# Kernel optimization log

Hardware: AMD Instinct MI355X
Metric: run time of the kernel (lower is better)

The kernel has to match this reference:

```python
import jax, jax.numpy as jnp
import numpy as np

D_MODEL = 1024
D_FF = 4096
NUM_EXPERTS = 8
TOP_K = 2
LN_EPS = 1e-5


def setup_inputs() -> dict:
    key = jax.random.key(0)
    ks = jax.random.split(key, 12)
    B, S, D, F, E = 4, 2048, D_MODEL, D_FF, NUM_EXPERTS
    s = 0.02
    return {
        "x": jax.random.normal(ks[0], (B, S, D), jnp.float32),
        # gating network: Linear(D, D//2) -> ReLU -> Linear(D//2, E)
        "gw1": jax.random.normal(ks[1], (D, D // 2), jnp.float32) * s,
        "gb1": jnp.zeros((D // 2,), jnp.float32),
        "gw2": jax.random.normal(ks[2], (D // 2, E), jnp.float32) * s,
        "gb2": jnp.zeros((E,), jnp.float32),
        # stacked expert FFNs: Linear(D,F) -> GELU -> Linear(F,D), then *scale + bias
        "we1": jax.random.normal(ks[3], (E, D, F), jnp.float32) * s,
        "be1": jnp.zeros((E, F), jnp.float32),
        "we2": jax.random.normal(ks[4], (E, F, D), jnp.float32) * s,
        "be2": jnp.zeros((E, D), jnp.float32),
        "escale": jnp.ones((E, D), jnp.float32),
        "ebias": jax.random.normal(ks[5], (E, D), jnp.float32) * 0.01,
        # output LayerNorm
        "gamma": jnp.ones((D,), jnp.float32),
        "beta": jnp.zeros((D,), jnp.float32),
    }


def _layernorm(x, gamma, beta):
    mu = jnp.mean(x, axis=-1, keepdims=True)
    var = jnp.mean(jnp.square(x - mu), axis=-1, keepdims=True)
    return (x - mu) * jax.lax.rsqrt(var + LN_EPS) * gamma + beta


def reference(x, gw1, gb1, gw2, gb2, we1, be1, we2, be2, escale, ebias, gamma, beta):
    B, S, D = x.shape
    xf = x.reshape(-1, D)  # [T, D]

    # ---- gating (eval mode: no noise, no dropout) ----
    gate_logits = jax.nn.relu(xf @ gw1 + gb1) @ gw2 + gb2  # [T, E]
    top_v, top_i = jax.lax.top_k(gate_logits, TOP_K)       # [T, K]
    gates = jax.nn.softmax(top_v, axis=-1)                 # [T, K]

    # load balancing loss: KL( uniform || mean softmax probs ), sum reduction
    probs = jax.nn.softmax(gate_logits, axis=-1)
    expert_probs = probs.mean(axis=0)                      # [E]
    t = 1.0 / NUM_EXPERTS
    load_loss = jnp.sum(t * (jnp.log(t) - jnp.log(expert_probs + 1e-8)))

    # ---- dense compute over ALL experts (faithful to source) ----
    h = jnp.einsum('td,edf->tef', xf, we1) + be1           # [T, E, F]
    h = jax.nn.gelu(h, approximate=False)                  # nn.GELU default = erf
    eo = jnp.einsum('tef,efd->ted', h, we2) + be2          # [T, E, D]
    eo = eo * escale + ebias                               # per-expert scale/bias

    # ---- top-k gather + weighted combine ----
    sel = jnp.take_along_axis(eo, top_i[:, :, None], axis=1)  # [T, K, D]
    out = jnp.sum(gates[:, :, None] * sel, axis=1)            # [T, D]

    y = _layernorm(x + out.reshape(B, S, D), gamma, beta)
    return y, load_loss
```

## Files before the change

kernel.cpp:

```cpp
#include <hip/hip_runtime.h>
#include <hip/hip_bf16.h>
#include <math.h>

#define T_TOK 8192
#define DM    1024
#define DFF   4096
#define NE    8
#define DH    512
#define NSLOT (T_TOK*2)
#define MAXT  136

typedef float  f32x4  __attribute__((ext_vector_type(4)));
typedef __bf16 bf16x8 __attribute__((ext_vector_type(8)));

__device__ inline ushort f2bf(float f) {
  union { float f; unsigned int u; } v; v.f = f;
  unsigned int r = (v.u + 0x7FFFu + ((v.u >> 16) & 1u)) >> 16;
  return (ushort)r;
}

__device__ inline float bf2f(ushort u) {
  union { unsigned int i; float f; } v; v.i = ((unsigned int)u) << 16; return v.f;
}

__device__ __forceinline__ float gelu_erf(float v) {
  float xx = v * 0.70710678118654752f;
  float ax = fabsf(xx);
  float t  = __builtin_amdgcn_rcpf(1.f + 0.3275911f * ax);
  float p  = t * (0.254829592f + t * (-0.284496736f + t * (1.421413741f +
             t * (-1.453152027f + t * 1.061405429f))));
  float er = 1.f - p * __expf(-ax * ax);
  er = copysignf(er, xx);
  return 0.5f * v * (1.f + er);
}

__device__ inline void gl_lds16(const void* g, void* l) {
  __builtin_amdgcn_global_load_lds(
      (const __attribute__((address_space(1))) unsigned int*)g,
      (__attribute__((address_space(3))) unsigned int*)l, 16, 0, 0);
}

__global__ void k_init(int* counts, int* fill, float* psum) {
  int i = threadIdx.x;
  if (i < NE) { counts[i] = 0; fill[i] = 0; psum[i] = 0.f; }
}

__global__ void k_cvt_x(const float* __restrict__ x, ushort* __restrict__ xh,
                        ushort* __restrict__ xl, int n4) {
  int i = blockIdx.x * blockDim.x + threadIdx.x;
  int st = gridDim.x * blockDim.x;
  for (; i < n4; i += st) {
    float4 v = ((const float4*)x)[i];
    ushort4 h, l;
    h.x = f2bf(v.x); l.x = f2bf(v.x - bf2f(h.x));
    h.y = f2bf(v.y); l.y = f2bf(v.y - bf2f(h.y));
    h.z = f2bf(v.z); l.z = f2bf(v.z - bf2f(h.z));
    h.w = f2bf(v.w); l.w = f2bf(v.w - bf2f(h.w));
    ((ushort4*)xh)[i] = h;
    ((ushort4*)xl)[i] = l;
  }
}

__global__ __launch_bounds__(256) void k_tr(const float* __restrict__ in,
                                            ushort* __restrict__ out, int R, int C) {
  __shared__ float tile[64][65];
  int e = blockIdx.z;
  in  += (size_t)e * R * C;
  out += (size_t)e * R * C;
  int r0 = blockIdx.y * 64, c0 = blockIdx.x * 64;
  int tx = threadIdx.x & 63, ty = threadIdx.x >> 6;
  for (int i = 0; i < 16; i++) {
    int r = ty + i * 4;
    tile[r][tx] = in[(size_t)(r0 + r) * C + c0 + tx];
  }
  __syncthreads();
  for (int i = 0; i < 16; i++) {
    int c = ty + i * 4;
    out[(size_t)(c0 + c) * R + r0 + tx] = f2bf(tile[tx][c]);
  }
}

__global__ __launch_bounds__(256) void k_trg(const float* __restrict__ in,
                                             ushort* __restrict__ outh,
                                             ushort* __restrict__ outl) {
  __shared__ float tile[64][65];
  int r0 = blockIdx.y * 64, c0 = blockIdx.x * 64;
  int tx = threadIdx.x & 63, ty = threadIdx.x >> 6;
  for (int i = 0; i < 16; i++) {
    int r = ty + i * 4;
    tile[r][tx] = in[(size_t)(r0 + r) * DH + c0 + tx];
  }
  __syncthreads();
  for (int i = 0; i < 16; i++) {
    int c = ty + i * 4;
    float f = tile[tx][c];
    ushort h = f2bf(f);
    outh[(size_t)(c0 + c) * DM + r0 + tx] = h;
    outl[(size_t)(c0 + c) * DM + r0 + tx] = f2bf(f - bf2f(h));
  }
}

__global__ __launch_bounds__(256) void k_gate1m(const ushort* __restrict__ xh,
                                                const ushort* __restrict__ xl,
                                                const ushort* __restrict__ w1ht,
                                                const ushort* __restrict__ w1lt,
                                                const float* __restrict__ b,
                                                float* __restrict__ g1) {
  constexpr int GX = DH / 128;
  constexpr int NWG = GX * (T_TOK / 128);
  int id = blockIdx.y * GX + blockIdx.x;
  int wg = (id & 7) * (NWG / 8) + (id >> 3);
  int m0 = (wg / GX) * 128;
  int n0 = (wg % GX) * 128;

  __shared__ ushort lds[2][16384];

  int t = threadIdx.x;
  int wave = t >> 6, lane = t & 63;
  int wr = wave >> 1, wc = wave & 1;

  int r = t >> 2;
  int csrc = (((t & 3) ^ ((t >> 3) & 3)) * 8);
  const ushort* ah0 = xh + (size_t)(m0 + r) * DM + csrc;
  const ushort* ah1 = xh + (size_t)(m0 + r + 64) * DM + csrc;
  const ushort* al0 = xl + (size_t)(m0 + r) * DM + csrc;
  const ushort* al1 = xl + (size_t)(m0 + r + 64) * DM + csrc;
  const ushort* bh0 = w1ht + (size_t)(n0 + r) * DM + csrc;
  const ushort* bh1 = w1ht + (size_t)(n0 + r + 64) * DM + csrc;
  const ushort* bl0 = w1lt + (size_t)(n0 + r) * DM + csrc;
  const ushort* bl1 = w1lt + (size_t)(n0 + r + 64) * DM + csrc;

  auto stage = [&](int b_, int k0) {
    ushort* base = lds[b_];
    gl_lds16(ah0 + k0, base + t * 8);
    gl_lds16(ah1 + k0, base + (t + 256) * 8);
    gl_lds16(al0 + k0, base + 4096 + t * 8);
    gl_lds16(al1 + k0, base + 4096 + (t + 256) * 8);
    gl_lds16(bh0 + k0, base + 8192 + t * 8);
    gl_lds16(bh1 + k0, base + 8192 + (t + 256) * 8);
    gl_lds16(bl0 + k0, base + 12288 + t * 8);
    gl_lds16(bl1 + k0, base + 12288 + (t + 256) * 8);
  };

  f32x4 acc[4][4] = {};
  int la = lane & 15;
  int kqs = (((lane >> 4) ^ ((la >> 1) & 3)) * 8);
  constexpr int NT = DM / 32;

  stage(0, 0);
  stage(1, 32);
  for (int kt = 0; kt < NT; kt++) {
    if (kt + 1 < NT) asm volatile("s_waitcnt vmcnt(8)" ::: "memory");
    else             asm volatile("s_waitcnt vmcnt(0)" ::: "memory");
    __builtin_amdgcn_s_barrier();
    const ushort* bb = lds[kt & 1];
    bf16x8 fah[4], fal[4], fbh[4], fbl[4];
#pragma unroll
    for (int m = 0; m < 4; m++) {
      int ro = (wr * 64 + m * 16 + la) * 32 + kqs;
      fah[m] = *(const bf16x8*)&bb[ro];
      fal[m] = *(const bf16x8*)&bb[4096 + ro];
    }
#pragma unroll
    for (int n = 0; n < 4; n++) {
      int ro = (wc * 64 + n * 16 + la) * 32 + kqs;
      fbh[n] = *(const bf16x8*)&bb[8192 + ro];
      fbl[n] = *(const bf16x8*)&bb[12288 + ro];
    }
    asm volatile("s_waitcnt lgkmcnt(0)" ::: "memory");
    __builtin_amdgcn_s_barrier();
    if (kt + 2 < NT) stage(kt & 1, (kt + 2) * 32);
#pragma unroll
    for (int m = 0; m < 4; m++)
#pragma unroll
      for (int n = 0; n < 4; n++)
        acc[m][n] = __builtin_amdgcn_mfma_f32_16x16x32_bf16(fah[m], fbh[n], acc[m][n], 0, 0, 0);
#pragma unroll
    for (int m = 0; m < 4; m++)
#pragma unroll
      for (int n = 0; n < 4; n++)
        acc[m][n] = __builtin_amdgcn_mfma_f32_16x16x32_bf16(fah[m], fbl[n], acc[m][n], 0, 0, 0);
#pragma unroll
    for (int m = 0; m < 4; m++)
#pragma unroll
      for (int n = 0; n < 4; n++)
        acc[m][n] = __builtin_amdgcn_mfma_f32_16x16x32_bf16(fal[m], fbh[n], acc[m][n], 0, 0, 0);
  }

#pragma unroll
  for (int m = 0; m < 4; m++) {
    int rbase = m0 + wr * 64 + m * 16 + ((lane >> 4) << 2);
#pragma unroll
    for (int n = 0; n < 4; n++) {
      int c = n0 + wc * 64 + n * 16 + la;
      float bv = b[c];
      f32x4 a = acc[m][n];
#pragma unroll
      for (int j = 0; j < 4; j++)
        g1[(size_t)(rbase + j) * DH + c] = fmaxf(a[j] + bv, 0.f);
    }
  }
}

__global__ __launch_bounds__(256) void k_gate2(const float* __restrict__ g1,
                                               const float* __restrict__ w2,
                                               const float* __restrict__ b2,
                                               float* __restrict__ logits) {
  int wave = threadIdx.x >> 6, lane = threadIdx.x & 63;
  int tok = blockIdx.x * 4 + wave;
  const float* row = &g1[(size_t)tok * DH];
  float v[8];
#pragma unroll
  for (int j = 0; j < 8; j++) v[j] = row[lane + 64 * j];
  float acc[8];
#pragma unroll
  for (int e = 0; e < NE; e++) {
    float s = 0.f;
#pragma unroll
    for (int j = 0; j < 8; j++) s += v[j] * w2[(size_t)(lane + 64 * j) * NE + e];
    acc[e] = s;
  }
  for (int off = 32; off > 0; off >>= 1)
#pragma unroll
    for (int e = 0; e < NE; e++) acc[e] += __shfl_down(acc[e], off);
  if (lane == 0)
#pragma unroll
    for (int e = 0; e < NE; e++) logits[(size_t)tok * NE + e] = acc[e] + b2[e];
}

__global__ __launch_bounds__(256) void k_route(const float* __restrict__ logits,
                                               int* __restrict__ topi,
                                               float* __restrict__ gatesw,
                                               int* __restrict__ counts,
                                               float* __restrict__ psum) {
  int t = blockIdx.x * blockDim.x + threadIdx.x;
  const float* lp = &logits[(size_t)t * NE];
  float l[8];
#pragma unroll
  for (int e = 0; e < NE; e++) l[e] = lp[e];
  int i0 = 0; float v0 = l[0];
#pragma unroll
  for (int e = 1; e < NE; e++) if (l[e] > v0) { v0 = l[e]; i0 = e; }
  int i1 = (i0 == 0) ? 1 : 0; float v1 = l[i1];
#pragma unroll
  for (int e = 0; e < NE; e++)
    if (e != i0 && l[e] > v1) { v1 = l[e]; i1 = e; }
  float g0 = 1.f / (1.f + expf(v1 - v0));
  topi[t * 2] = i0; topi[t * 2 + 1] = i1;
  gatesw[t * 2] = g0; gatesw[t * 2 + 1] = 1.f - g0;
  float p[8]; float s = 0.f;
#pragma unroll
  for (int e = 0; e < NE; e++) { p[e] = expf(l[e] - v0); s += p[e]; }
  float inv = 1.f / s;
  int lane = threadIdx.x & 63;
#pragma unroll
  for (int e = 0; e < NE; e++) {
    float pe = p[e] * inv;
    for (int off = 32; off > 0; off >>= 1) pe += __shfl_down(pe, off);
    if (lane == 0) atomicAdd(&psum[e], pe);
  }
#pragma unroll
  for (int e = 0; e < NE; e++) {
    unsigned long long m0 = __ballot(i0 == e);
    unsigned long long m1 = __ballot(i1 == e);
    if (lane == 0) {
      int c = __popcll(m0) + __popcll(m1);
      if (c) atomicAdd(&counts[e], c);
    }
  }
}

__global__ void k_scan(const int* __restrict__ counts, int* __restrict__ offsets,
                       const float* __restrict__ psum, float* __restrict__ loss_out,
                       int* __restrict__ tile_e, int* __restrict__ tile_mt) {
  if (threadIdx.x == 0) {
    int off = 0;
    for (int e = 0; e < NE; e++) { offsets[e] = off; off += counts[e]; }
    offsets[NE] = off;
    float tt = 1.f / NE, loss = 0.f;
    for (int e = 0; e < NE; e++) {
      float pe = psum[e] / (float)T_TOK;
      loss += tt * (logf(tt) - logf(pe + 1e-8f));
    }
    loss_out[0] = loss;
    int n = 0;
    for (int e = 0; e < NE; e++) {
      int rows = counts[e];
      for (int mt = 0; mt * 128 < rows; mt++) { tile_e[n] = e; tile_mt[n] = mt; n++; }
    }
    for (int i = n; i < MAXT; i++) { tile_e[i] = -1; tile_mt[i] = 0; }
  }
}

__global__ __launch_bounds__(256) void k_fill(const int* __restrict__ topi,
                                              const int* __restrict__ offsets,
                                              int* __restrict__ fill,
                                              int* __restrict__ slot_tok,
                                              int* __restrict__ tok_slot) {
  int t = blockIdx.x * blockDim.x + threadIdx.x;
  for (int k = 0; k < 2; k++) {
    int e = topi[t * 2 + k];
    int pos = offsets[e] + atomicAdd(&fill[e], 1);
    slot_tok[pos] = t;
    tok_slot[t * 2 + k] = pos;
  }
}

__global__ __launch_bounds__(256, 3) void k_egemm1(const ushort* __restrict__ xb,
                                                   const ushort* __restrict__ w1t,
                                                   const float* __restrict__ be1,
                                                   const int* __restrict__ slot_tok,
                                                   const int* __restrict__ offsets,
                                                   const int* __restrict__ tile_e,
                                                   const int* __restrict__ tile_mt,
                                                   ushort* __restrict__ H) {
  constexpr int GX = DFF / 128;
  constexpr int NWG = GX * MAXT;
  int id = blockIdx.y * GX + blockIdx.x;
  int wg = (id & 7) * (NWG / 8) + (id >> 3);
  int ty = wg / GX;
  int n0 = (wg % GX) * 128;
  int e = tile_e[ty];
  if (e < 0) return;
  int mt = tile_mt[ty];
  int beg = offsets[e], nrows = offsets[e + 1] - beg;
  const ushort* B = w1t + (size_t)e * DFF * DM;

  __shared__ ushort As[2][4096];
  __shared__ ushort Bs[2][4096];

  int t = threadIdx.x;
  int wave = t >> 6, lane = t & 63;
  int wr = wave >> 1, wc = wave & 1;

  int r_g0 = mt * 128 + (t >> 2);
  int r_g1 = r_g0 + 64;
  int tok0 = slot_tok[beg + (r_g0 < nrows ? r_g0 : 0)];
  int tok1 = slot_tok[beg + (r_g1 < nrows ? r_g1 : 0)];
  int acol = (((t & 3) ^ ((t >> 3) & 3)) * 8);
  const ushort* aptr0 = xb + (size_t)tok0 * DM + acol;
  const ushort* aptr1 = xb + (size_t)tok1 * DM + acol;
  const ushort* bptr0 = B + (size_t)(n0 + (t >> 2)) * DM + acol;
  const ushort* bptr1 = B + (size_t)(n0 + (t >> 2) + 64) * DM + acol;
  char* adst = (char*)As + t * 16;
  char* bdst = (char*)Bs + t * 16;

  auto stage = [&](int b, int k0) {
    gl_lds16(aptr0 + k0, adst + b * 8192);
    gl_lds16(aptr1 + k0, adst + b * 8192 + 4096);
    gl_lds16(bptr0 + k0, bdst + b * 8192);
    gl_lds16(bptr1 + k0, bdst + b * 8192 + 4096);
  };

  f32x4 acc[4][4] = {};
  int la = lane & 15;
  int kqs = (((lane >> 4) ^ ((la >> 1) & 3)) * 8);
  constexpr int NT = DM / 32;

  stage(0, 0);
  stage(1, 32);
  for (int kt = 0; kt < NT; kt++) {
    if (kt + 1 < NT) asm volatile("s_waitcnt vmcnt(4)" ::: "memory");
    else             asm volatile("s_waitcnt vmcnt(0)" ::: "memory");
    __builtin_amdgcn_s_barrier();
    const ushort* Ab = As[kt & 1];
    const ushort* Bb = Bs[kt & 1];
    bf16x8 af[4], bfr[4];
#pragma unroll
    for (int m = 0; m < 4; m++)
      af[m] = *(const bf16x8*)&Ab[(wr * 64 + m * 16 + la) * 32 + kqs];
#pragma unroll
    for (int n = 0; n < 4; n++)
      bfr[n] = *(const bf16x8*)&Bb[(wc * 64 + n * 16 + la) * 32 + kqs];
    asm volatile("s_waitcnt lgkmcnt(0)" ::: "memory");
    __builtin_amdgcn_s_barrier();
    if (kt + 2 < NT) stage(kt & 1, (kt + 2) * 32);
#pragma unroll
    for (int m = 0; m < 4; m++)
#pragma unroll
      for (int n = 0; n < 4; n++)
        acc[m][n] = __builtin_amdgcn_mfma_f32_16x16x32_bf16(af[m], bfr[n], acc[m][n], 0, 0, 0);
  }

  int row0 = mt * 128 + wr * 64;
  int c_of = n0 + wc * 64;
#pragma unroll
  for (int m = 0; m < 4; m++) {
    int rbase = row0 + m * 16 + ((lane >> 4) << 2);
#pragma unroll
    for (int n = 0; n < 4; n++) {
      int c = c_of + n * 16 + la;
      float b1 = be1[e * DFF + c];
      f32x4 a = acc[m][n];
#pragma unroll
      for (int j = 0; j < 4; j++) {
        int rr = rbase + j;
        if (rr < nrows) {
          float v = a[j] + b1;
          H[(size_t)(beg + rr) * DFF + c] = f2bf(gelu_erf(v));
        }
      }
    }
  }
}

__global__ __launch_bounds__(256, 3) void k_egemm2(const ushort* __restrict__ H,
                                                   const ushort* __restrict__ w2t,
                                                   const float* __restrict__ be2,
                                                   const float* __restrict__ escale,
                                                   const float* __restrict__ ebias,
                                                   const int* __restrict__ offsets,
                                                   const int* __restrict__ tile_e,
                                                   const int* __restrict__ tile_mt,
                                                   ushort* __restrict__ eo) {
  constexpr int GX = DM / 128;
  constexpr int NWG = GX * MAXT;
  int id = blockIdx.y * GX + blockIdx.x;
  int wg = (id & 7) * (NWG / 8) + (id >> 3);
  int ty = wg / GX;
  int n0 = (wg % GX) * 128;
  int e = tile_e[ty];
  if (e < 0) return;
  int mt = tile_mt[ty];
  int beg = offsets[e], nrows = offsets[e + 1] - beg;
  const ushort* B = w2t + (size_t)e * DM * DFF;

  __shared__ ushort As[2][4096];
  __shared__ ushort Bs[2][4096];

  int t = threadIdx.x;
  int wave = t >> 6, lane = t & 63;
  int wr = wave >> 1, wc = wave & 1;

  int r_g0 = mt * 128 + (t >> 2);
  int r_g1 = r_g0 + 64;
  int s0 = beg + (r_g0 < nrows ? r_g0 : 0);
  int s1 = beg + (r_g1 < nrows ? r_g1 : 0);
  int acol = (((t & 3) ^ ((t >> 3) & 3)) * 8);
  const ushort* aptr0 = H + (size_t)s0 * DFF + acol;
  const ushort* aptr1 = H + (size_t)s1 * DFF + acol;
  const ushort* bptr0 = B + (size_t)(n0 + (t >> 2)) * DFF + acol;
  const ushort* bptr1 = B + (size_t)(n0 + (t >> 2) + 64) * DFF + acol;
  char* adst = (char*)As + t * 16;
  char* bdst = (char*)Bs + t * 16;

  auto stage = [&](int b, int k0) {
    gl_lds16(aptr0 + k0, adst + b * 8192);
    gl_lds16(aptr1 + k0, adst + b * 8192 + 4096);
    gl_lds16(bptr0 + k0, bdst + b * 8192);
    gl_lds16(bptr1 + k0, bdst + b * 8192 + 4096);
  };

  f32x4 acc[4][4] = {};
  int la = lane & 15;
  int kqs = (((lane >> 4) ^ ((la >> 1) & 3)) * 8);
  constexpr int NT = DFF / 32;

  stage(0, 0);
  stage(1, 32);
  for (int kt = 0; kt < NT; kt++) {
    if (kt + 1 < NT) asm volatile("s_waitcnt vmcnt(4)" ::: "memory");
    else             asm volatile("s_waitcnt vmcnt(0)" ::: "memory");
    __builtin_amdgcn_s_barrier();
    const ushort* Ab = As[kt & 1];
    const ushort* Bb = Bs[kt & 1];
    bf16x8 af[4], bfr[4];
#pragma unroll
    for (int m = 0; m < 4; m++)
      af[m] = *(const bf16x8*)&Ab[(wr * 64 + m * 16 + la) * 32 + kqs];
#pragma unroll
    for (int n = 0; n < 4; n++)
      bfr[n] = *(const bf16x8*)&Bb[(wc * 64 + n * 16 + la) * 32 + kqs];
    asm volatile("s_waitcnt lgkmcnt(0)" ::: "memory");
    __builtin_amdgcn_s_barrier();
    if (kt + 2 < NT) stage(kt & 1, (kt + 2) * 32);
#pragma unroll
    for (int m = 0; m < 4; m++)
#pragma unroll
      for (int n = 0; n < 4; n++)
        acc[m][n] = __builtin_amdgcn_mfma_f32_16x16x32_bf16(af[m], bfr[n], acc[m][n], 0, 0, 0);
  }

  int row0 = mt * 128 + wr * 64;
  int c_of = n0 + wc * 64;
#pragma unroll
  for (int m = 0; m < 4; m++) {
    int rbase = row0 + m * 16 + ((lane >> 4) << 2);
#pragma unroll
    for (int n = 0; n < 4; n++) {
      int c = c_of + n * 16 + la;
      float b2 = be2[e * DM + c];
      float sc = escale[e * DM + c];
      float bb = ebias[e * DM + c];
      f32x4 a = acc[m][n];
#pragma unroll
      for (int j = 0; j < 4; j++) {
        int rr = rbase + j;
        if (rr < nrows) {
          float v = (a[j] + b2) * sc + bb;
          eo[(size_t)(beg + rr) * DM + c] = f2bf(v);
        }
      }
    }
  }
}

__global__ __launch_bounds__(256) void k_ln(const float* __restrict__ x,
                                            const ushort* __restrict__ eo,
                                            const int* __restrict__ tok_slot,
                                            const float* __restrict__ gatesw,
                                            const float* __restrict__ gamma,
                                            const float* __restrict__ beta,
                                            float* __restrict__ y) {
  int t = blockIdx.x;
  int s0 = tok_slot[t * 2], s1 = tok_slot[t * 2 + 1];
  float g0 = gatesw[t * 2], g1 = gatesw[t * 2 + 1];
  const float* xr = &x[(size_t)t * DM];
  const ushort* e0 = &eo[(size_t)s0 * DM];
  const ushort* e1 = &eo[(size_t)s1 * DM];
  int tid = threadIdx.x;
  int c0 = tid * 4;
  float4 xv = *(const float4*)&xr[c0];
  ushort4 a0 = *(const ushort4*)&e0[c0];
  ushort4 a1 = *(const ushort4*)&e1[c0];
  float v[4];
  v[0] = xv.x + g0 * bf2f(a0.x) + g1 * bf2f(a1.x);
  v[1] = xv.y + g0 * bf2f(a0.y) + g1 * bf2f(a1.y);
  v[2] = xv.z + g0 * bf2f(a0.z) + g1 * bf2f(a1.z);
  v[3] = xv.w + g0 * bf2f(a0.w) + g1 * bf2f(a1.w);
  float sum = v[0] + v[1] + v[2] + v[3];
  __shared__ float red[4];
  __shared__ float red2[4];
  for (int off = 32; off > 0; off >>= 1) sum += __shfl_down(sum, off);
  if ((tid & 63) == 0) red[tid >> 6] = sum;
  __syncthreads();
  float mu = (red[0] + red[1] + red[2] + red[3]) * (1.f / DM);
  float vs = 0.f;
#pragma unroll
  for (int i = 0; i < 4; i++) { float d = v[i] - mu; vs += d * d; }
  for (int off = 32; off > 0; off >>= 1) vs += __shfl_down(vs, off);
  if ((tid & 63) == 0) red2[tid >> 6] = vs;
  __syncthreads();
  float var = (red2[0] + red2[1] + red2[2] + red2[3]) * (1.f / DM);
  float rs = rsqrtf(var + 1e-5f);
  float4 gm = *(const float4*)&gamma[c0];
  float4 bt = *(const float4*)&beta[c0];
  float4 o;
  o.x = (v[0] - mu) * rs * gm.x + bt.x;
  o.y = (v[1] - mu) * rs * gm.y + bt.y;
  o.z = (v[2] - mu) * rs * gm.z + bt.z;
  o.w = (v[3] - mu) * rs * gm.w + bt.w;
  *(float4*)&y[(size_t)t * DM + c0] = o;
}

extern "C" void kernel_launch(void* const* d_in, const int* in_sizes, int n_in,
                              void* d_out, int out_size, void* d_ws, size_t ws_size,
                              hipStream_t stream) {
  const float* x    = (const float*)d_in[0];
  const float* gw1  = (const float*)d_in[1];
  const float* gb1  = (const float*)d_in[2];
  const float* gw2  = (const float*)d_in[3];
  const float* gb2  = (const float*)d_in[4];
  const float* we1  = (const float*)d_in[5];
  const float* be1  = (const float*)d_in[6];
  const float* we2  = (const float*)d_in[7];
  const float* be2  = (const float*)d_in[8];
  const float* escale = (const float*)d_in[9];
  const float* ebias  = (const float*)d_in[10];
  const float* gamma  = (const float*)d_in[11];
  const float* beta   = (const float*)d_in[12];
  float* y = (float*)d_out;
  float* loss_out = y + (size_t)T_TOK * DM;

  char* w = (char*)d_ws;
  ushort* xh    = (ushort*)w; w += (size_t)T_TOK * DM * 2;
  ushort* xl    = (ushort*)w; w += (size_t)T_TOK * DM * 2;
  ushort* w1t   = (ushort*)w; w += (size_t)NE * DFF * DM * 2;
  ushort* w2t   = (ushort*)w; w += (size_t)NE * DM * DFF * 2;
  ushort* H     = (ushort*)w; w += (size_t)NSLOT * DFF * 2;
  ushort* eo    = (ushort*)w; w += (size_t)NSLOT * DM * 2;
  ushort* w1ht  = (ushort*)w; w += (size_t)DH * DM * 2;
  ushort* w1lt  = (ushort*)w; w += (size_t)DH * DM * 2;
  float* g1     = (float*)w;  w += (size_t)T_TOK * DH * 4;
  float* logits = (float*)w;  w += (size_t)T_TOK * NE * 4;
  int*   topi   = (int*)w;    w += (size_t)T_TOK * 2 * 4;
  float* gatesw = (float*)w;  w += (size_t)T_TOK * 2 * 4;
  int* slot_tok = (int*)w;    w += (size_t)NSLOT * 4;
  int* tok_slot = (int*)w;    w += (size_t)T_TOK * 2 * 4;
  int* counts   = (int*)w;    w += 64;
  int* fill     = (int*)w;    w += 64;
  int* offsets  = (int*)w;    w += 64;
  float* psum   = (float*)w;  w += 64;
  int* tile_e   = (int*)w;    w += MAXT * 4 + 32;
  int* tile_mt  = (int*)w;    w += MAXT * 4 + 32;

  k_init<<<1, 64, 0, stream>>>(counts, fill, psum);
  k_cvt_x<<<2048, 256, 0, stream>>>(x, xh, xl, T_TOK * DM / 4);
  k_trg<<<dim3(8, 16), 256, 0, stream>>>(gw1, w1ht, w1lt);
  k_tr<<<dim3(64, 16, 8), 256, 0, stream>>>(we1, w1t, DM, DFF);
  k_tr<<<dim3(16, 64, 8), 256, 0, stream>>>(we2, w2t, DFF, DM);
  k_gate1m<<<dim3(DH / 128, T_TOK / 128), 256, 0, stream>>>(xh, xl, w1ht, w1lt, gb1, g1);
  k_gate2<<<T_TOK / 4, 256, 0, stream>>>(g1, gw2, gb2, logits);
  k_route<<<T_TOK / 256, 256, 0, stream>>>(logits, topi, gatesw, counts, psum);
  k_scan<<<1, 64, 0, stream>>>(counts, offsets, psum, loss_out, tile_e, tile_mt);
  k_fill<<<T_TOK / 256, 256, 0, stream>>>(topi, offsets, fill, slot_tok, tok_slot);
  k_egemm1<<<dim3(DFF / 128, MAXT), 256, 0, stream>>>(xh, w1t, be1, slot_tok, offsets,
                                                      tile_e, tile_mt, H);
  k_egemm2<<<dim3(DM / 128, MAXT), 256, 0, stream>>>(H, w2t, be2, escale, ebias,
                                                     offsets, tile_e, tile_mt, eo);
  k_ln<<<T_TOK, 256, 0, stream>>>(x, eo, tok_slot, gatesw, gamma, beta, y);
}
```

Baseline: 688.8 us.

## Enlarge expert GEMM1 tiles, triple-buffer LDS, vectorize transposes, fold init kernel

The first expert GEMM now uses 256x256 tiles with 512 threads and a separate coarser tile schedule, which raises operand reuse per workgroup. Both expert GEMMs move to a three-stage LDS ring with a single barrier per k-step and raise wave priority around the MFMA block. The weight-transpose kernel now uses float4 loads and ushort4 stores, and the counter-init kernel is folded into the x conversion kernel to save a launch. In exchange, GEMM1 has fewer workgroups, more registers per thread and a larger LDS footprint, which may lower occupancy and waste more work on padded rows.

Measured after the change: 754.2 us. 1.09x slower.

```diff
diff --git a/kernel.cpp b/kernel.cpp
--- a/kernel.cpp
+++ b/kernel.cpp
@@ -9,6 +9,7 @@
 #define DH    512
 #define NSLOT (T_TOK*2)
 #define MAXT  136
+#define MAXT2 72
 
 typedef float  f32x4  __attribute__((ext_vector_type(4)));
 typedef __bf16 bf16x8 __attribute__((ext_vector_type(8)));
@@ -40,13 +41,14 @@
       (__attribute__((address_space(3))) unsigned int*)l, 16, 0, 0);
 }
 
-__global__ void k_init(int* counts, int* fill, float* psum) {
-  int i = threadIdx.x;
-  if (i < NE) { counts[i] = 0; fill[i] = 0; psum[i] = 0.f; }
-}
+#define SBAR  __builtin_amdgcn_s_barrier()
 
 __global__ void k_cvt_x(const float* __restrict__ x, ushort* __restrict__ xh,
-                        ushort* __restrict__ xl, int n4) {
+                        ushort* __restrict__ xl, int n4,
+                        int* counts, int* fill, float* psum) {
+  if (blockIdx.x == 0 && threadIdx.x < NE) {
+    counts[threadIdx.x] = 0; fill[threadIdx.x] = 0; psum[threadIdx.x] = 0.f;
+  }
   int i = blockIdx.x * blockDim.x + threadIdx.x;
   int st = gridDim.x * blockDim.x;
   for (; i < n4; i += st) {
@@ -68,15 +70,25 @@
   in  += (size_t)e * R * C;
   out += (size_t)e * R * C;
   int r0 = blockIdx.y * 64, c0 = blockIdx.x * 64;
-  int tx = threadIdx.x & 63, ty = threadIdx.x >> 6;
-  for (int i = 0; i < 16; i++) {
-    int r = ty + i * 4;
-    tile[r][tx] = in[(size_t)(r0 + r) * C + c0 + tx];
+  int t = threadIdx.x;
+  int lr = t >> 4, lc = (t & 15) * 4;
+#pragma unroll
+  for (int i = 0; i < 4; i++) {
+    int r = lr + i * 16;
+    float4 v = *(const float4*)&in[(size_t)(r0 + r) * C + c0 + lc];
+    tile[r][lc] = v.x; tile[r][lc + 1] = v.y; tile[r][lc + 2] = v.z; tile[r][lc + 3] = v.w;
   }
   __syncthreads();
-  for (int i = 0; i < 16; i++) {
-    int c = ty + i * 4;
-    out[(size_t)(c0 + c) * R + r0 + tx] = f2bf(tile[tx][c]);
+  int g = t & 15, cc = t >> 4;
+#pragma unroll
+  for (int i = 0; i < 4; i++) {
+    int c = cc + i * 16;
+    ushort4 o;
+    o.x = f2bf(tile[g * 4 + 0][c]);
+    o.y = f2bf(tile[g * 4 + 1][c]);
+    o.z = f2bf(tile[g * 4 + 2][c]);
+    o.w = f2bf(tile[g * 4 + 3][c]);
+    *(ushort4*)&out[(size_t)(c0 + c) * R + r0 + g * 4] = o;
   }
 }
 
@@ -272,7 +284,8 @@
 
 __global__ void k_scan(const int* __restrict__ counts, int* __restrict__ offsets,
                        const float* __restrict__ psum, float* __restrict__ loss_out,
-                       int* __restrict__ tile_e, int* __restrict__ tile_mt) {
+                       int* __restrict__ tile_e, int* __restrict__ tile_mt,
+                       int* __restrict__ tile_e2, int* __restrict__ tile_mt2) {
   if (threadIdx.x == 0) {
     int off = 0;
     for (int e = 0; e < NE; e++) { offsets[e] = off; off += counts[e]; }
@@ -289,6 +302,12 @@
       for (int mt = 0; mt * 128 < rows; mt++) { tile_e[n] = e; tile_mt[n] = mt; n++; }
     }
     for (int i = n; i < MAXT; i++) { tile_e[i] = -1; tile_mt[i] = 0; }
+    n = 0;
+    for (int e = 0; e < NE; e++) {
+      int rows = counts[e];
+      for (int mt = 0; mt * 256 < rows; mt++) { tile_e2[n] = e; tile_mt2[n] = mt; n++; }
+    }
+    for (int i = n; i < MAXT2; i++) { tile_e2[i] = -1; tile_mt2[i] = 0; }
   }
 }
 
@@ -306,99 +325,97 @@
   }
 }
 
-__global__ __launch_bounds__(256, 3) void k_egemm1(const ushort* __restrict__ xb,
+__global__ __launch_bounds__(512, 2) void k_egemm1(const ushort* __restrict__ xb,
                                                    const ushort* __restrict__ w1t,
                                                    const float* __restrict__ be1,
                                                    const int* __restrict__ slot_tok,
                                                    const int* __restrict__ offsets,
-                                                   const int* __restrict__ tile_e,
-                                                   const int* __restrict__ tile_mt,
+                                                   const int* __restrict__ tile_e2,
+                                                   const int* __restrict__ tile_mt2,
                                                    ushort* __restrict__ H) {
-  constexpr int GX = DFF / 128;
-  constexpr int NWG = GX * MAXT;
+  constexpr int GX = DFF / 256;
+  constexpr int NWG = GX * MAXT2;
+  constexpr int NT = DM / 32;
   int id = blockIdx.y * GX + blockIdx.x;
   int wg = (id & 7) * (NWG / 8) + (id >> 3);
   int ty = wg / GX;
-  int n0 = (wg % GX) * 128;
-  int e = tile_e[ty];
+  int n0c = (wg % GX) * 256;
+  int e = tile_e2[ty];
   if (e < 0) return;
-  int mt = tile_mt[ty];
+  int mt = tile_mt2[ty];
   int beg = offsets[e], nrows = offsets[e + 1] - beg;
-  const ushort* B = w1t + (size_t)e * DFF * DM;
-
-  __shared__ ushort As[2][4096];
-  __shared__ ushort Bs[2][4096];
+  const ushort* Bw = w1t + (size_t)e * DFF * DM;
+
+  __shared__ ushort As[3][8192];
+  __shared__ ushort Bs[3][8192];
 
   int t = threadIdx.x;
-  int wave = t >> 6, lane = t & 63;
-  int wr = wave >> 1, wc = wave & 1;
-
-  int r_g0 = mt * 128 + (t >> 2);
-  int r_g1 = r_g0 + 64;
-  int tok0 = slot_tok[beg + (r_g0 < nrows ? r_g0 : 0)];
-  int tok1 = slot_tok[beg + (r_g1 < nrows ? r_g1 : 0)];
-  int acol = (((t & 3) ^ ((t >> 3) & 3)) * 8);
-  const ushort* aptr0 = xb + (size_t)tok0 * DM + acol;
-  const ushort* aptr1 = xb + (size_t)tok1 * DM + acol;
-  const ushort* bptr0 = B + (size_t)(n0 + (t >> 2)) * DM + acol;
-  const ushort* bptr1 = B + (size_t)(n0 + (t >> 2) + 64) * DM + acol;
+  int lane = t & 63, la = lane & 15, lh = lane >> 4;
+  int wid = t >> 6, wm = wid >> 2, wn = wid & 3;
+
+  int csrc = (((t & 3) ^ ((t >> 3) & 3)) * 8);
+  auto arow = [&](int r) {
+    r = mt * 256 + r; if (r >= nrows) r = nrows - 1;
+    return (size_t)slot_tok[beg + r];
+  };
+  int rr0 = t >> 2;
+  const ushort* aptr0 = xb + arow(rr0) * DM + csrc;
+  const ushort* aptr1 = xb + arow(128 + rr0) * DM + csrc;
+  const ushort* bptr0 = Bw + (size_t)(n0c + rr0) * DM + csrc;
+  const ushort* bptr1 = Bw + (size_t)(n0c + 128 + rr0) * DM + csrc;
   char* adst = (char*)As + t * 16;
   char* bdst = (char*)Bs + t * 16;
 
   auto stage = [&](int b, int k0) {
-    gl_lds16(aptr0 + k0, adst + b * 8192);
-    gl_lds16(aptr1 + k0, adst + b * 8192 + 4096);
-    gl_lds16(bptr0 + k0, bdst + b * 8192);
-    gl_lds16(bptr1 + k0, bdst + b * 8192 + 4096);
+    gl_lds16(aptr0 + k0, adst + b * 16384);
+    gl_lds16(aptr1 + k0, adst + b * 16384 + 8192);
+    gl_lds16(bptr0 + k0, bdst + b * 16384);
+    gl_lds16(bptr1 + k0, bdst + b * 16384 + 8192);
   };
 
-  f32x4 acc[4][4] = {};
-  int la = lane & 15;
+  f32x4 acc[8][4] = {};
   int kqs = (((lane >> 4) ^ ((la >> 1) & 3)) * 8);
-  constexpr int NT = DM / 32;
 
   stage(0, 0);
   stage(1, 32);
+  asm volatile("s_waitcnt vmcnt(4)" ::: "memory");
+  SBAR;
   for (int kt = 0; kt < NT; kt++) {
-    if (kt + 1 < NT) asm volatile("s_waitcnt vmcnt(4)" ::: "memory");
-    else             asm volatile("s_waitcnt vmcnt(0)" ::: "memory");
-    __builtin_amdgcn_s_barrier();
-    const ushort* Ab = As[kt & 1];
-    const ushort* Bb = Bs[kt & 1];
-    bf16x8 af[4], bfr[4];
-#pragma unroll
-    for (int m = 0; m < 4; m++)
-      af[m] = *(const bf16x8*)&Ab[(wr * 64 + m * 16 + la) * 32 + kqs];
+    if (kt + 2 < NT) stage((kt + 2) % 3, (kt + 2) * 32);
+    const ushort* Ab = As[kt % 3];
+    const ushort* Bb = Bs[kt % 3];
+    bf16x8 af[8], bfr[4];
+#pragma unroll
+    for (int m = 0; m < 8; m++)
+      af[m] = *(const bf16x8*)&Ab[(wm * 128 + m * 16 + la) * 32 + kqs];
 #pragma unroll
     for (int n = 0; n < 4; n++)
-      bfr[n] = *(const bf16x8*)&Bb[(wc * 64 + n * 16 + la) * 32 + kqs];
+      bfr[n] = *(const bf16x8*)&Bb[(wn * 64 + n * 16 + la) * 32 + kqs];
     asm volatile("s_waitcnt lgkmcnt(0)" ::: "memory");
-    __builtin_amdgcn_s_barrier();
-    if (kt + 2 < NT) stage(kt & 1, (kt + 2) * 32);
-#pragma unroll
-    for (int m = 0; m < 4; m++)
+    __builtin_amdgcn_s_setprio(1);
+#pragma unroll
+    for (int m = 0; m < 8; m++)
 #pragma unroll
       for (int n = 0; n < 4; n++)
         acc[m][n] = __builtin_amdgcn_mfma_f32_16x16x32_bf16(af[m], bfr[n], acc[m][n], 0, 0, 0);
-  }
-
-  int row0 = mt * 128 + wr * 64;
-  int c_of = n0 + wc * 64;
-#pragma unroll
-  for (int m = 0; m < 4; m++) {
-    int rbase = row0 + m * 16 + ((lane >> 4) << 2);
+    __builtin_amdgcn_s_setprio(0);
+    if (kt + 2 < NT)      { asm volatile("s_waitcnt vmcnt(4)" ::: "memory"); SBAR; }
+    else if (kt + 1 < NT) { asm volatile("s_waitcnt vmcnt(0)" ::: "memory"); SBAR; }
+  }
+
+#pragma unroll
+  for (int m = 0; m < 8; m++) {
+    int lrow = mt * 256 + wm * 128 + m * 16 + lh * 4;
 #pragma unroll
     for (int n = 0; n < 4; n++) {
-      int c = c_of + n * 16 + la;
+      int c = n0c + wn * 64 + n * 16 + la;
       float b1 = be1[e * DFF + c];
       f32x4 a = acc[m][n];
 #pragma unroll
       for (int j = 0; j < 4; j++) {
-        int rr = rbase + j;
-        if (rr < nrows) {
-          float v = a[j] + b1;
-          H[(size_t)(beg + rr) * DFF + c] = f2bf(gelu_erf(v));
-        }
+        int rr = lrow + j;
+        if (rr < nrows)
+          H[(size_t)(beg + rr) * DFF + c] = f2bf(gelu_erf(a[j] + b1));
       }
     }
   }
@@ -425,8 +442,8 @@
   int beg = offsets[e], nrows = offsets[e + 1] - beg;
   const ushort* B = w2t + (size_t)e * DM * DFF;
 
-  __shared__ ushort As[2][4096];
-  __shared__ ushort Bs[2][4096];
+  __shared__ ushort As[3][4096];
+  __shared__ ushort Bs[3][4096];
 
   int t = threadIdx.x;
   int wave = t >> 6, lane = t & 63;
@@ -458,12 +475,12 @@
 
   stage(0, 0);
   stage(1, 32);
+  asm volatile("s_waitcnt vmcnt(4)" ::: "memory");
+  SBAR;
   for (int kt = 0; kt < NT; kt++) {
-    if (kt + 1 < NT) asm volatile("s_waitcnt vmcnt(4)" ::: "memory");
-    else             asm volatile("s_waitcnt vmcnt(0)" ::: "memory");
-    __builtin_amdgcn_s_barrier();
-    const ushort* Ab = As[kt & 1];
-    const ushort* Bb = Bs[kt & 1];
+    if (kt + 2 < NT) stage((kt + 2) % 3, (kt + 2) * 32);
+    const ushort* Ab = As[kt % 3];
+    const ushort* Bb = Bs[kt % 3];
     bf16x8 af[4], bfr[4];
 #pragma unroll
     for (int m = 0; m < 4; m++)
@@ -472,13 +489,15 @@
     for (int n = 0; n < 4; n++)
       bfr[n] = *(const bf16x8*)&Bb[(wc * 64 + n * 16 + la) * 32 + kqs];
     asm volatile("s_waitcnt lgkmcnt(0)" ::: "memory");
-    __builtin_amdgcn_s_barrier();
-    if (kt + 2 < NT) stage(kt & 1, (kt + 2) * 32);
+    __builtin_amdgcn_s_setprio(1);
 #pragma unroll
     for (int m = 0; m < 4; m++)
 #pragma unroll
       for (int n = 0; n < 4; n++)
         acc[m][n] = __builtin_amdgcn_mfma_f32_16x16x32_bf16(af[m], bfr[n], acc[m][n], 0, 0, 0);
+    __builtin_amdgcn_s_setprio(0);
+    if (kt + 2 < NT)      { asm volatile("s_waitcnt vmcnt(4)" ::: "memory"); SBAR; }
+    else if (kt + 1 < NT) { asm volatile("s_waitcnt vmcnt(0)" ::: "memory"); SBAR; }
   }
 
   int row0 = mt * 128 + wr * 64;
@@ -593,19 +612,21 @@
   float* psum   = (float*)w;  w += 64;
   int* tile_e   = (int*)w;    w += MAXT * 4 + 32;
   int* tile_mt  = (int*)w;    w += MAXT * 4 + 32;
-
-  k_init<<<1, 64, 0, stream>>>(counts, fill, psum);
-  k_cvt_x<<<2048, 256, 0, stream>>>(x, xh, xl, T_TOK * DM / 4);
+  int* tile_e2  = (int*)w;    w += MAXT2 * 4 + 32;
+  int* tile_mt2 = (int*)w;    w += MAXT2 * 4 + 32;
+
+  k_cvt_x<<<2048, 256, 0, stream>>>(x, xh, xl, T_TOK * DM / 4, counts, fill, psum);
   k_trg<<<dim3(8, 16), 256, 0, stream>>>(gw1, w1ht, w1lt);
   k_tr<<<dim3(64, 16, 8), 256, 0, stream>>>(we1, w1t, DM, DFF);
   k_tr<<<dim3(16, 64, 8), 256, 0, stream>>>(we2, w2t, DFF, DM);
   k_gate1m<<<dim3(DH / 128, T_TOK / 128), 256, 0, stream>>>(xh, xl, w1ht, w1lt, gb1, g1);
   k_gate2<<<T_TOK / 4, 256, 0, stream>>>(g1, gw2, gb2, logits);
   k_route<<<T_TOK / 256, 256, 0, stream>>>(logits, topi, gatesw, counts, psum);
-  k_scan<<<1, 64, 0, stream>>>(counts, offsets, psum, loss_out, tile_e, tile_mt);
+  k_scan<<<1, 64, 0, stream>>>(counts, offsets, psum, loss_out, tile_e, tile_mt,
+                               tile_e2, tile_mt2);
   k_fill<<<T_TOK / 256, 256, 0, stream>>>(topi, offsets, fill, slot_tok, tok_slot);
-  k_egemm1<<<dim3(DFF / 128, MAXT), 256, 0, stream>>>(xh, w1t, be1, slot_tok, offsets,
-                                                      tile_e, tile_mt, H);
+  k_egemm1<<<dim3(DFF / 256, MAXT2), 512, 0, stream>>>(xh, w1t, be1, slot_tok, offsets,
+                                                       tile_e2, tile_mt2, H);
   k_egemm2<<<dim3(DM / 128, MAXT), 256, 0, stream>>>(H, w2t, be2, escale, ebias,
                                                      offsets, tile_e, tile_mt, eo);
   k_ln<<<T_TOK, 256, 0, stream>>>(x, eo, tok_slot, gatesw, gamma, beta, y);
```
